# Optimization experiments

Hardware: AMD Instinct MI355X
Metric: run time of the kernel (lower is better)

## Reference

```python
import jax, jax.numpy as jnp
import numpy as np

EPS_RMS = 1.1920929e-07  # torch.finfo(float32).eps, RMSNorm default when eps=None
EPS_BN = 1e-5            # BatchNorm1d default eps
NUM_CODES = 4096
EMBED_DIM = 64


def rms_norm(x):
    # nn.RMSNorm(embed_dim, elementwise_affine=False)
    ms = jnp.mean(x * x, axis=-1, keepdims=True)
    return x * jax.lax.rsqrt(ms + EPS_RMS)


def get_codebook(codebook_weight, bn_weight, bn_bias):
    # BatchNorm1d with track_running_stats=False: batch stats over codebook rows
    mean = jnp.mean(codebook_weight, axis=0)
    var = jnp.var(codebook_weight, axis=0)  # biased variance, as torch BN uses
    h = (codebook_weight - mean) * jax.lax.rsqrt(var + EPS_BN) * bn_weight + bn_bias
    return rms_norm(h)


def setup_inputs() -> dict:
    key = jax.random.key(0)
    k1, k2 = jax.random.split(key)
    z = jax.random.normal(k1, (8, 4096, EMBED_DIM), dtype=jnp.float32)
    # codebook init: uniform(-1/num_codes, 1/num_codes)
    codebook_weight = jax.random.uniform(
        k2, (NUM_CODES, EMBED_DIM), dtype=jnp.float32,
        minval=-1.0 / NUM_CODES, maxval=1.0 / NUM_CODES)
    bn_weight = jnp.ones((EMBED_DIM,), dtype=jnp.float32)
    bn_bias = jnp.zeros((EMBED_DIM,), dtype=jnp.float32)
    return {"z": z, "codebook_weight": codebook_weight,
            "bn_weight": bn_weight, "bn_bias": bn_bias}


def reference(z, codebook_weight, bn_weight, bn_bias):
    # c_in / c_out are Identity since width == embed_dim
    z_e = rms_norm(z)                                   # [B, S, D]
    cb = get_codebook(codebook_weight, bn_weight, bn_bias)  # [K, D]

    z_flat = z_e.reshape(-1, z_e.shape[-1])             # [N, D]
    # argmin of cdist == argmin of squared distance (sqrt is monotone)
    d2 = (jnp.sum(z_flat * z_flat, axis=1, keepdims=True)
          - 2.0 * (z_flat @ cb.T)
          + jnp.sum(cb * cb, axis=1))                   # [N, K]
    q = jnp.argmin(d2, axis=1)                          # [N]

    z_q = cb[q].reshape(z_e.shape)                      # gather codes
    q = q.reshape(z_e.shape[:-1])

    # straight-through: gradient flows to z_e only
    z_q_st = z_e + jax.lax.stop_gradient(z_q - z_e)
    # ret_dict entries: 'z' (detached z_e), 'q', 'z_q' (detached)
    return (z_q_st, jax.lax.stop_gradient(z_e), q, jax.lax.stop_gradient(z_q))
```

## Files before the change

kernel.cpp:

```cpp
#include <hip/hip_runtime.h>
#include <math.h>

#define NROWS 32768
#define DIM   64
#define NCODE 4096
#define EPS_RMS 1.1920929e-07f
#define EPS_BN  1e-5f

typedef _Float16 f16x8 __attribute__((ext_vector_type(8)));
typedef float    f32x4 __attribute__((ext_vector_type(4)));

#define WS_PS   0
#define WS_PQ   16384
#define WS_CC   32768
#define WS_CB32 49152
#define WS_CH   (49152 + 1048576)
#define WS_CL   (WS_CH + 524288)

#define OUT1 ((size_t)NROWS * DIM)
#define OUT2 ((size_t)2 * NROWS * DIM)
#define OUT3 (OUT2 + NROWS)

#define MFMA16(a, b, c) __builtin_amdgcn_mfma_f32_16x16x32_f16(a, b, c, 0, 0, 0)

__device__ __forceinline__ void async_copy16(void* lds, const void* g) {
    __builtin_amdgcn_global_load_lds(
        (const __attribute__((address_space(1))) unsigned int*)g,
        (__attribute__((address_space(3))) unsigned int*)lds, 16, 0, 0);
}

__global__ __launch_bounds__(256) void k_bn1(const float* __restrict__ w,
                                             char* __restrict__ wsb) {
    __shared__ float s1[4][64], s2[4][64];
    int lane = threadIdx.x & 63, v = threadIdx.x >> 6;
    long base = (long)blockIdx.x * 64 + v * 16;
    float s = 0.f, sq = 0.f;
    #pragma unroll
    for (int i = 0; i < 16; i++) {
        float x = w[(base + i) * DIM + lane];
        s += x; sq += x * x;
    }
    s1[v][lane] = s; s2[v][lane] = sq;
    __syncthreads();
    if (threadIdx.x < 64) {
        float ts = s1[0][lane] + s1[1][lane] + s1[2][lane] + s1[3][lane];
        float tq = s2[0][lane] + s2[1][lane] + s2[2][lane] + s2[3][lane];
        ((float*)(wsb + WS_PS))[blockIdx.x * 64 + lane] = ts;
        ((float*)(wsb + WS_PQ))[blockIdx.x * 64 + lane] = tq;
    }
}

__global__ __launch_bounds__(256) void k_cb(const float* __restrict__ w,
                                            const float* __restrict__ bnw,
                                            const float* __restrict__ bnb,
                                            char* __restrict__ wsb) {
    __shared__ float s1[4][64], s2[4][64], af[64], bf[64];
    int t = threadIdx.x, lane = t & 63, v = t >> 6;
    const float* ps = (const float*)(wsb + WS_PS);
    const float* pq = (const float*)(wsb + WS_PQ);
    float s = 0.f, sq = 0.f;
    #pragma unroll
    for (int b = 0; b < 16; b++) {
        s  += ps[(v * 16 + b) * 64 + lane];
        sq += pq[(v * 16 + b) * 64 + lane];
    }
    s1[v][lane] = s; s2[v][lane] = sq;
    __syncthreads();
    if (t < 64) {
        float ts = s1[0][lane] + s1[1][lane] + s1[2][lane] + s1[3][lane];
        float tq = s2[0][lane] + s2[1][lane] + s2[2][lane] + s2[3][lane];
        float mean = ts * (1.0f / NCODE);
        float var  = tq * (1.0f / NCODE) - mean * mean;
        float a = rsqrtf(var + EPS_BN) * bnw[lane];
        af[lane] = a;
        bf[lane] = bnb[lane] - mean * a;
    }
    __syncthreads();
    float a = af[lane], bb = bf[lane];
    float*     cb32 = (float*)(wsb + WS_CB32);
    _Float16*  chG  = (_Float16*)(wsb + WS_CH);
    _Float16*  clG  = (_Float16*)(wsb + WS_CL);
    float*     ccp  = (float*)(wsb + WS_CC);
    #pragma unroll
    for (int i = 0; i < 4; i++) {
        long row = (long)blockIdx.x * 16 + v * 4 + i;
        float x = w[row * DIM + lane];
        float h = fmaf(x, a, bb);
        float ss = h * h;
        #pragma unroll
        for (int m = 1; m < 64; m <<= 1) ss += __shfl_xor(ss, m);
        float rms = rsqrtf(ss * (1.0f / DIM) + EPS_RMS);
        float c = h * rms;
        cb32[row * DIM + lane] = c;
        _Float16 ch = (_Float16)c;
        chG[row * DIM + lane] = ch;
        clG[row * DIM + lane] = (_Float16)(c - (float)ch);
        float cs = c * c;
        #pragma unroll
        for (int m = 1; m < 64; m <<= 1) cs += __shfl_xor(cs, m);
        if (lane == 0) ccp[row] = cs;
    }
}

__global__ __launch_bounds__(256, 2) void k_main(const float* __restrict__ z,
                                                 const char* __restrict__ wsb,
                                                 float* __restrict__ out) {
    __shared__ __align__(16) unsigned char sm[32768];
    unsigned char* chT = sm;
    unsigned char* clT = sm + 16384;

    const int tid  = threadIdx.x;
    const int lane = tid & 63;
    const int w    = tid >> 6;
    const int wr   = w >> 1;
    const int wc   = w & 1;
    const int l15  = lane & 15;
    const int l4   = lane >> 4;
    const long rowbase = (long)blockIdx.x * 64;

    const _Float16* chG  = (const _Float16*)(wsb + WS_CH);
    const _Float16* clG  = (const _Float16*)(wsb + WS_CL);
    const float*    ccG  = (const float*)(wsb + WS_CC);
    const float*    cb32 = (const float*)(wsb + WS_CB32);

    {
        int r = tid >> 2, seg = tid & 3;
        const float* zrow = z + (rowbase + r) * DIM + seg * 16;
        float vv[16];
        float ss = 0.f;
        #pragma unroll
        for (int i = 0; i < 16; i++) { vv[i] = zrow[i]; ss += vv[i] * vv[i]; }
        ss += __shfl_xor(ss, 1);
        ss += __shfl_xor(ss, 2);
        float rms = rsqrtf(ss * (1.0f / DIM) + EPS_RMS);
        float* oz = out + OUT1 + (rowbase + r) * DIM + seg * 16;
        __align__(16) _Float16 hb[16], lb[16];
        #pragma unroll
        for (int i = 0; i < 16; i++) {
            float x = vv[i] * rms;
            oz[i] = x;
            _Float16 h = (_Float16)x;
            hb[i] = h;
            lb[i] = (_Float16)(x - (float)h);
        }
        unsigned char* zhp = sm + r * 128 + seg * 32;
        unsigned char* zlp = sm + 8192 + r * 128 + seg * 32;
        ((f16x8*)zhp)[0] = ((f16x8*)hb)[0];
        ((f16x8*)zhp)[1] = ((f16x8*)hb)[1];
        ((f16x8*)zlp)[0] = ((f16x8*)lb)[0];
        ((f16x8*)zlp)[1] = ((f16x8*)lb)[1];
    }
    __syncthreads();

    f16x8 ah[2][2], al[2][2];
    #pragma unroll
    for (int s = 0; s < 2; s++)
        #pragma unroll
        for (int c = 0; c < 2; c++) {
            int arow = wr * 32 + s * 16 + l15;
            ah[s][c] = *(const f16x8*)(sm + arow * 128 + c * 64 + l4 * 16);
            al[s][c] = *(const f16x8*)(sm + 8192 + arow * 128 + c * 64 + l4 * 16);
        }
    __syncthreads();

    float bd[2][4];
    int   bix[2][4];
    #pragma unroll
    for (int s = 0; s < 2; s++)
        #pragma unroll
        for (int r = 0; r < 4; r++) { bd[s][r] = 3.4e38f; bix[s][r] = 0; }

    for (int p = 0; p < 32; ++p) {
        int cbase = p * 128;
        #pragma unroll
        for (int i = 0; i < 4; i++) {
            int B = w * 4096 + i * 1024 + lane * 16;
            int code = B >> 7;
            int sp   = (B >> 4) & 7;
            long ge = (long)(cbase + code) * DIM + (long)((sp ^ (code & 7)) * 8);
            async_copy16(chT + w * 4096 + i * 1024, chG + ge);
            async_copy16(clT + w * 4096 + i * 1024, clG + ge);
        }
        float ccv[4];
        #pragma unroll
        for (int q = 0; q < 4; q++)
            ccv[q] = ccG[cbase + wc * 64 + q * 16 + l15];
        __syncthreads();

        #pragma unroll 2
        for (int q = 0; q < 4; q++) {
            int ccol = wc * 64 + q * 16;
            int coderow = ccol + l15;
            f16x8 bh[2], bl[2];
            #pragma unroll
            for (int c = 0; c < 2; c++) {
                int byte = coderow * 128 + ((c * 64 + l4 * 16) ^ ((coderow & 7) << 4));
                bh[c] = *(const f16x8*)(chT + byte);
                bl[c] = *(const f16x8*)(clT + byte);
            }
            #pragma unroll
            for (int s = 0; s < 2; s++) {
                f32x4 acc = {0.f, 0.f, 0.f, 0.f};
                acc = MFMA16(ah[s][0], bh[0], acc);
                acc = MFMA16(ah[s][1], bh[1], acc);
                acc = MFMA16(ah[s][0], bl[0], acc);
                acc = MFMA16(ah[s][1], bl[1], acc);
                acc = MFMA16(al[s][0], bh[0], acc);
                acc = MFMA16(al[s][1], bh[1], acc);
                int code = cbase + ccol + l15;
                #pragma unroll
                for (int r = 0; r < 4; r++) {
                    float cand = fmaf(-2.0f, acc[r], ccv[q]);
                    if (cand < bd[s][r]) { bd[s][r] = cand; bix[s][r] = code; }
                }
            }
        }
        __syncthreads();
    }

    float* redd = (float*)sm;
    int*   redi = (int*)(sm + 512);
    int*   bidx = (int*)(sm + 1024);
    #pragma unroll
    for (int s = 0; s < 2; s++)
        #pragma unroll
        for (int r = 0; r < 4; r++) {
            float d = bd[s][r];
            int   ix = bix[s][r];
            #pragma unroll
            for (int m = 1; m < 16; m <<= 1) {
                float od = __shfl_xor(d, m);
                int   oi = __shfl_xor(ix, m);
                if (od < d || (od == d && oi < ix)) { d = od; ix = oi; }
            }
            if (l15 == 0) {
                int rowloc = wr * 32 + s * 16 + l4 * 4 + r;
                redd[rowloc * 2 + wc] = d;
                redi[rowloc * 2 + wc] = ix;
            }
        }
    __syncthreads();
    if (tid < 64) {
        float d0 = redd[tid * 2 + 0], d1 = redd[tid * 2 + 1];
        int   i0 = redi[tid * 2 + 0], i1 = redi[tid * 2 + 1];
        int ix = (d1 < d0 || (d1 == d0 && i1 < i0)) ? i1 : i0;
        bidx[tid] = ix;
        out[OUT2 + rowbase + tid] = (float)ix;
    }
    __syncthreads();
    {
        int r = tid >> 2, seg = tid & 3;
        int ix = bidx[r];
        const float* src = cb32 + (long)ix * DIM + seg * 16;
        float* o0 = out + (rowbase + r) * DIM + seg * 16;
        float* o3 = out + OUT3 + (rowbase + r) * DIM + seg * 16;
        #pragma unroll
        for (int i = 0; i < 16; i++) { float t = src[i]; o0[i] = t; o3[i] = t; }
    }
}

extern "C" void kernel_launch(void* const* d_in, const int* in_sizes, int n_in,
                              void* d_out, int out_size, void* d_ws, size_t ws_size,
                              hipStream_t stream) {
    const float* z   = (const float*)d_in[0];
    const float* w   = (const float*)d_in[1];
    const float* bnw = (const float*)d_in[2];
    const float* bnb = (const float*)d_in[3];
    float* out = (float*)d_out;
    char*  wsb = (char*)d_ws;

    k_bn1 <<<64,   256, 0, stream>>>(w, wsb);
    k_cb  <<<256,  256, 0, stream>>>(w, bnw, bnb, wsb);
    k_main<<<512,  256, 0, stream>>>(z, wsb, out);
}
```

Before: 84.37 us.

## Double-buffer codebook tiles in LDS and fold the code-norm term into MFMA

The main kernel now keeps two 32 KB LDS buffers for the fp16 hi/lo codebook tiles. It issues async copies for tile p+1, and its norm values, before computing on tile p, so global-to-LDS transfer overlaps the MFMA work and one barrier per iteration goes away. The distance is rewritten as an argmax of dot minus half the code norm, with the scaled norm precomputed by the codebook kernel and used as the MFMA accumulator initializer. The six-MFMA dependency chain is split into two independent chains, and the swizzled LDS offsets are hoisted out of the loop. LDS use per block doubles to 64 KB, which may reduce how many blocks fit per CU.

New measurement: 87.66 us. 3.9% more time.

```diff
diff --git a/kernel.cpp b/kernel.cpp
--- a/kernel.cpp
+++ b/kernel.cpp
@@ -98,16 +98,14 @@
         float cs = c * c;
         #pragma unroll
         for (int m = 1; m < 64; m <<= 1) cs += __shfl_xor(cs, m);
-        if (lane == 0) ccp[row] = cs;
+        if (lane == 0) ccp[row] = -0.5f * cs;
     }
 }
 
 __global__ __launch_bounds__(256, 2) void k_main(const float* __restrict__ z,
                                                  const char* __restrict__ wsb,
                                                  float* __restrict__ out) {
-    __shared__ __align__(16) unsigned char sm[32768];
-    unsigned char* chT = sm;
-    unsigned char* clT = sm + 16384;
+    __shared__ __align__(16) unsigned char sm[65536];
 
     const int tid  = threadIdx.x;
     const int lane = tid & 63;
@@ -120,8 +118,22 @@
 
     const _Float16* chG  = (const _Float16*)(wsb + WS_CH);
     const _Float16* clG  = (const _Float16*)(wsb + WS_CL);
-    const float*    ccG  = (const float*)(wsb + WS_CC);
+    const float*    ccnG = (const float*)(wsb + WS_CC);
     const float*    cb32 = (const float*)(wsb + WS_CB32);
+
+    const int B0    = w * 4096 + lane * 16;
+    const int scode = B0 >> 7;
+    const int ssp   = (B0 >> 4) & 7;
+    const long gsw  = (long)scode * DIM + (long)((ssp ^ (scode & 7)) * 8);
+
+    #pragma unroll
+    for (int i = 0; i < 4; i++) {
+        async_copy16(sm + B0 + i * 1024,         chG + gsw + i * 8 * DIM / 8 * 8);
+    }
+    #pragma unroll
+    for (int i = 0; i < 4; i++) {
+        async_copy16(sm + 16384 + B0 + i * 1024, clG + gsw + i * 8 * DIM / 8 * 8);
+    }
 
     {
         int r = tid >> 2, seg = tid & 3;
@@ -143,8 +155,8 @@
             hb[i] = h;
             lb[i] = (_Float16)(x - (float)h);
         }
-        unsigned char* zhp = sm + r * 128 + seg * 32;
-        unsigned char* zlp = sm + 8192 + r * 128 + seg * 32;
+        unsigned char* zhp = sm + 32768 + r * 128 + seg * 32;
+        unsigned char* zlp = sm + 40960 + r * 128 + seg * 32;
         ((f16x8*)zhp)[0] = ((f16x8*)hb)[0];
         ((f16x8*)zhp)[1] = ((f16x8*)hb)[1];
         ((f16x8*)zlp)[0] = ((f16x8*)lb)[0];
@@ -158,64 +170,82 @@
         #pragma unroll
         for (int c = 0; c < 2; c++) {
             int arow = wr * 32 + s * 16 + l15;
-            ah[s][c] = *(const f16x8*)(sm + arow * 128 + c * 64 + l4 * 16);
-            al[s][c] = *(const f16x8*)(sm + 8192 + arow * 128 + c * 64 + l4 * 16);
-        }
-    __syncthreads();
-
-    float bd[2][4];
+            ah[s][c] = *(const f16x8*)(sm + 32768 + arow * 128 + c * 64 + l4 * 16);
+            al[s][c] = *(const f16x8*)(sm + 40960 + arow * 128 + c * 64 + l4 * 16);
+        }
+    __syncthreads();
+
+    int boff[4][2];
+    #pragma unroll
+    for (int q = 0; q < 4; q++) {
+        int coderow = wc * 64 + q * 16 + l15;
+        #pragma unroll
+        for (int c = 0; c < 2; c++)
+            boff[q][c] = coderow * 128 + ((c * 64 + l4 * 16) ^ ((coderow & 7) << 4));
+    }
+
+    float ccv[4];
+    #pragma unroll
+    for (int q = 0; q < 4; q++)
+        ccv[q] = ccnG[wc * 64 + q * 16 + l15];
+
+    float bmax[2][4];
     int   bix[2][4];
     #pragma unroll
     for (int s = 0; s < 2; s++)
         #pragma unroll
-        for (int r = 0; r < 4; r++) { bd[s][r] = 3.4e38f; bix[s][r] = 0; }
+        for (int r = 0; r < 4; r++) { bmax[s][r] = -3.4e38f; bix[s][r] = 0; }
 
     for (int p = 0; p < 32; ++p) {
-        int cbase = p * 128;
-        #pragma unroll
-        for (int i = 0; i < 4; i++) {
-            int B = w * 4096 + i * 1024 + lane * 16;
-            int code = B >> 7;
-            int sp   = (B >> 4) & 7;
-            long ge = (long)(cbase + code) * DIM + (long)((sp ^ (code & 7)) * 8);
-            async_copy16(chT + w * 4096 + i * 1024, chG + ge);
-            async_copy16(clT + w * 4096 + i * 1024, clG + ge);
-        }
-        float ccv[4];
-        #pragma unroll
-        for (int q = 0; q < 4; q++)
-            ccv[q] = ccG[cbase + wc * 64 + q * 16 + l15];
-        __syncthreads();
+        float ccn_nx[4];
+        if (p + 1 < 32) {
+            const float* cn = ccnG + (p + 1) * 128;
+            #pragma unroll
+            for (int q = 0; q < 4; q++)
+                ccn_nx[q] = cn[wc * 64 + q * 16 + l15];
+            unsigned char* nb = sm + ((p + 1) & 1) * 32768;
+            const _Float16* gh = chG + (long)(p + 1) * 128 * DIM + gsw;
+            const _Float16* gl = clG + (long)(p + 1) * 128 * DIM + gsw;
+            #pragma unroll
+            for (int i = 0; i < 4; i++)
+                async_copy16(nb + B0 + i * 1024,         gh + i * 512);
+            #pragma unroll
+            for (int i = 0; i < 4; i++)
+                async_copy16(nb + 16384 + B0 + i * 1024, gl + i * 512);
+        }
+
+        const unsigned char* chT = sm + (p & 1) * 32768;
+        const unsigned char* clT = chT + 16384;
 
         #pragma unroll 2
         for (int q = 0; q < 4; q++) {
-            int ccol = wc * 64 + q * 16;
-            int coderow = ccol + l15;
             f16x8 bh[2], bl[2];
             #pragma unroll
             for (int c = 0; c < 2; c++) {
-                int byte = coderow * 128 + ((c * 64 + l4 * 16) ^ ((coderow & 7) << 4));
-                bh[c] = *(const f16x8*)(chT + byte);
-                bl[c] = *(const f16x8*)(clT + byte);
+                bh[c] = *(const f16x8*)(chT + boff[q][c]);
+                bl[c] = *(const f16x8*)(clT + boff[q][c]);
             }
+            int code = p * 128 + wc * 64 + q * 16 + l15;
+            f32x4 ci = {ccv[q], ccv[q], ccv[q], ccv[q]};
             #pragma unroll
             for (int s = 0; s < 2; s++) {
-                f32x4 acc = {0.f, 0.f, 0.f, 0.f};
-                acc = MFMA16(ah[s][0], bh[0], acc);
-                acc = MFMA16(ah[s][1], bh[1], acc);
-                acc = MFMA16(ah[s][0], bl[0], acc);
-                acc = MFMA16(ah[s][1], bl[1], acc);
-                acc = MFMA16(al[s][0], bh[0], acc);
-                acc = MFMA16(al[s][1], bh[1], acc);
-                int code = cbase + ccol + l15;
+                f32x4 a0 = MFMA16(ah[s][0], bh[0], ci);
+                a0 = MFMA16(ah[s][0], bl[0], a0);
+                a0 = MFMA16(al[s][0], bh[0], a0);
+                f32x4 zz = {0.f, 0.f, 0.f, 0.f};
+                f32x4 a1 = MFMA16(ah[s][1], bh[1], zz);
+                a1 = MFMA16(ah[s][1], bl[1], a1);
+                a1 = MFMA16(al[s][1], bh[1], a1);
                 #pragma unroll
                 for (int r = 0; r < 4; r++) {
-                    float cand = fmaf(-2.0f, acc[r], ccv[q]);
-                    if (cand < bd[s][r]) { bd[s][r] = cand; bix[s][r] = code; }
+                    float v = a0[r] + a1[r];
+                    if (v > bmax[s][r]) { bmax[s][r] = v; bix[s][r] = code; }
                 }
             }
         }
         __syncthreads();
+        #pragma unroll
+        for (int q = 0; q < 4; q++) ccv[q] = ccn_nx[q];
     }
 
     float* redd = (float*)sm;
@@ -225,13 +255,13 @@
     for (int s = 0; s < 2; s++)
         #pragma unroll
         for (int r = 0; r < 4; r++) {
-            float d = bd[s][r];
+            float d = bmax[s][r];
             int   ix = bix[s][r];
             #pragma unroll
             for (int m = 1; m < 16; m <<= 1) {
                 float od = __shfl_xor(d, m);
                 int   oi = __shfl_xor(ix, m);
-                if (od < d || (od == d && oi < ix)) { d = od; ix = oi; }
+                if (od > d || (od == d && oi < ix)) { d = od; ix = oi; }
             }
             if (l15 == 0) {
                 int rowloc = wr * 32 + s * 16 + l4 * 4 + r;
@@ -243,7 +273,7 @@
     if (tid < 64) {
         float d0 = redd[tid * 2 + 0], d1 = redd[tid * 2 + 1];
         int   i0 = redi[tid * 2 + 0], i1 = redi[tid * 2 + 1];
-        int ix = (d1 < d0 || (d1 == d0 && i1 < i0)) ? i1 : i0;
+        int ix = (d1 > d0 || (d1 == d0 && i1 < i0)) ? i1 : i0;
         bidx[tid] = ix;
         out[OUT2 + rowbase + tid] = (float)ix;
     }
@@ -269,7 +299,7 @@
     float* out = (float*)d_out;
     char*  wsb = (char*)d_ws;
 
-    k_bn1 <<<64,   256, 0, stream>>>(w, wsb);
-    k_cb  <<<256,  256, 0, stream>>>(w, bnw, bnb, wsb);
-    k_main<<<512,  256, 0, stream>>>(z, wsb, out);
-}
+    k_bn1 <<<64,  256, 0, stream>>>(w, wsb);
+    k_cb  <<<256, 256, 0, stream>>>(w, bnw, bnb, wsb);
+    k_main<<<512, 256, 0, stream>>>(z, wsb, out);
+}
```

## Prepack codebook into MFMA fragment layout and stream from global per wave

Applied to the files above, without the earlier changes.

The codebook kernel now writes fp16 hi/lo codes already arranged in MFMA B-fragment order, along with a precomputed -0.5*||c||^2 bias. The main kernel drops the LDS staging loop and its per-tile barriers. Each wave loads its fragments straight from global memory with double-buffered registers, covering 1024 codes for all 64 rows, and seeds the accumulator with the bias so it can take a running max. This removes LDS traffic and synchronisation and raises occupancy to 3 blocks per SM. In exchange, each wave re-reads the codebook from L2 for every block, and per-thread register use rises. The z and gather I/O is also vectorised to float4.

Measured after the change: 70.26 us (median of 2 runs). -16.7%, faster.

```diff
diff --git a/kernel.cpp b/kernel.cpp
--- a/kernel.cpp
+++ b/kernel.cpp
@@ -14,20 +14,14 @@
 #define WS_PQ   16384
 #define WS_CC   32768
 #define WS_CB32 49152
-#define WS_CH   (49152 + 1048576)
-#define WS_CL   (WS_CH + 524288)
+#define WS_PH   (49152 + 1048576)
+#define WS_PL   (WS_PH + 524288)
 
 #define OUT1 ((size_t)NROWS * DIM)
 #define OUT2 ((size_t)2 * NROWS * DIM)
 #define OUT3 (OUT2 + NROWS)
 
 #define MFMA16(a, b, c) __builtin_amdgcn_mfma_f32_16x16x32_f16(a, b, c, 0, 0, 0)
-
-__device__ __forceinline__ void async_copy16(void* lds, const void* g) {
-    __builtin_amdgcn_global_load_lds(
-        (const __attribute__((address_space(1))) unsigned int*)g,
-        (__attribute__((address_space(3))) unsigned int*)lds, 16, 0, 0);
-}
 
 __global__ __launch_bounds__(256) void k_bn1(const float* __restrict__ w,
                                              char* __restrict__ wsb) {
@@ -55,6 +49,7 @@
                                             const float* __restrict__ bnb,
                                             char* __restrict__ wsb) {
     __shared__ float s1[4][64], s2[4][64], af[64], bf[64];
+    __shared__ _Float16 sh[16][64], sl[16][64];
     int t = threadIdx.x, lane = t & 63, v = t >> 6;
     const float* ps = (const float*)(wsb + WS_PS);
     const float* pq = (const float*)(wsb + WS_PQ);
@@ -77,13 +72,13 @@
     }
     __syncthreads();
     float a = af[lane], bb = bf[lane];
-    float*     cb32 = (float*)(wsb + WS_CB32);
-    _Float16*  chG  = (_Float16*)(wsb + WS_CH);
-    _Float16*  clG  = (_Float16*)(wsb + WS_CL);
-    float*     ccp  = (float*)(wsb + WS_CC);
+    float* cb32 = (float*)(wsb + WS_CB32);
+    float* ccp  = (float*)(wsb + WS_CC);
+    int g = blockIdx.x;
     #pragma unroll
     for (int i = 0; i < 4; i++) {
-        long row = (long)blockIdx.x * 16 + v * 4 + i;
+        int  rl  = v * 4 + i;
+        long row = (long)g * 16 + rl;
         float x = w[row * DIM + lane];
         float h = fmaf(x, a, bb);
         float ss = h * h;
@@ -93,169 +88,185 @@
         float c = h * rms;
         cb32[row * DIM + lane] = c;
         _Float16 ch = (_Float16)c;
-        chG[row * DIM + lane] = ch;
-        clG[row * DIM + lane] = (_Float16)(c - (float)ch);
+        sh[rl][lane] = ch;
+        sl[rl][lane] = (_Float16)(c - (float)ch);
         float cs = c * c;
         #pragma unroll
         for (int m = 1; m < 64; m <<= 1) cs += __shfl_xor(cs, m);
-        if (lane == 0) ccp[row] = cs;
-    }
-}
-
-__global__ __launch_bounds__(256, 2) void k_main(const float* __restrict__ z,
+        if (lane == 0) ccp[row] = -0.5f * cs;
+    }
+    __syncthreads();
+    {
+        int u = t & 127;
+        int c = u >> 6, l = u & 63;
+        int codel = l & 15;
+        int kbase = c * 32 + (l >> 4) * 8;
+        size_t dst = (size_t)((g * 2 + c) * 64 + l) * 16;
+        if (t < 128) {
+            *(f16x8*)(wsb + WS_PH + dst) = *(const f16x8*)&sh[codel][kbase];
+        } else {
+            *(f16x8*)(wsb + WS_PL + dst) = *(const f16x8*)&sl[codel][kbase];
+        }
+    }
+}
+
+__global__ __launch_bounds__(256, 3) void k_main(const float* __restrict__ z,
                                                  const char* __restrict__ wsb,
                                                  float* __restrict__ out) {
-    __shared__ __align__(16) unsigned char sm[32768];
-    unsigned char* chT = sm;
-    unsigned char* clT = sm + 16384;
+    __shared__ __align__(16) unsigned char sm[18688];
 
     const int tid  = threadIdx.x;
     const int lane = tid & 63;
     const int w    = tid >> 6;
-    const int wr   = w >> 1;
-    const int wc   = w & 1;
     const int l15  = lane & 15;
     const int l4   = lane >> 4;
     const long rowbase = (long)blockIdx.x * 64;
 
-    const _Float16* chG  = (const _Float16*)(wsb + WS_CH);
-    const _Float16* clG  = (const _Float16*)(wsb + WS_CL);
-    const float*    ccG  = (const float*)(wsb + WS_CC);
-    const float*    cb32 = (const float*)(wsb + WS_CB32);
+    const float* ccnG = (const float*)(wsb + WS_CC);
+    const float* cb32 = (const float*)(wsb + WS_CB32);
 
     {
         int r = tid >> 2, seg = tid & 3;
-        const float* zrow = z + (rowbase + r) * DIM + seg * 16;
-        float vv[16];
+        const float4* zp = (const float4*)(z + (rowbase + r) * DIM + seg * 16);
+        float4 v4[4];
         float ss = 0.f;
         #pragma unroll
-        for (int i = 0; i < 16; i++) { vv[i] = zrow[i]; ss += vv[i] * vv[i]; }
+        for (int i = 0; i < 4; i++) {
+            v4[i] = zp[i];
+            ss += v4[i].x * v4[i].x + v4[i].y * v4[i].y + v4[i].z * v4[i].z + v4[i].w * v4[i].w;
+        }
         ss += __shfl_xor(ss, 1);
         ss += __shfl_xor(ss, 2);
         float rms = rsqrtf(ss * (1.0f / DIM) + EPS_RMS);
-        float* oz = out + OUT1 + (rowbase + r) * DIM + seg * 16;
+        float4* oz = (float4*)(out + OUT1 + (rowbase + r) * DIM + seg * 16);
         __align__(16) _Float16 hb[16], lb[16];
         #pragma unroll
-        for (int i = 0; i < 16; i++) {
-            float x = vv[i] * rms;
-            oz[i] = x;
-            _Float16 h = (_Float16)x;
-            hb[i] = h;
-            lb[i] = (_Float16)(x - (float)h);
+        for (int i = 0; i < 4; i++) {
+            float xs[4] = {v4[i].x, v4[i].y, v4[i].z, v4[i].w};
+            #pragma unroll
+            for (int j = 0; j < 4; j++) {
+                float x = xs[j] * rms;
+                _Float16 h = (_Float16)x;
+                hb[i * 4 + j] = h;
+                lb[i * 4 + j] = (_Float16)(x - (float)h);
+                xs[j] = x;
+            }
+            oz[i] = make_float4(xs[0], xs[1], xs[2], xs[3]);
         }
         unsigned char* zhp = sm + r * 128 + seg * 32;
-        unsigned char* zlp = sm + 8192 + r * 128 + seg * 32;
         ((f16x8*)zhp)[0] = ((f16x8*)hb)[0];
         ((f16x8*)zhp)[1] = ((f16x8*)hb)[1];
+        unsigned char* zlp = zhp + 8192;
         ((f16x8*)zlp)[0] = ((f16x8*)lb)[0];
         ((f16x8*)zlp)[1] = ((f16x8*)lb)[1];
     }
     __syncthreads();
 
-    f16x8 ah[2][2], al[2][2];
-    #pragma unroll
-    for (int s = 0; s < 2; s++)
+    f16x8 ah[4][2], al[4][2];
+    #pragma unroll
+    for (int s = 0; s < 4; s++)
         #pragma unroll
         for (int c = 0; c < 2; c++) {
-            int arow = wr * 32 + s * 16 + l15;
-            ah[s][c] = *(const f16x8*)(sm + arow * 128 + c * 64 + l4 * 16);
-            al[s][c] = *(const f16x8*)(sm + 8192 + arow * 128 + c * 64 + l4 * 16);
-        }
-    __syncthreads();
-
-    float bd[2][4];
-    int   bix[2][4];
-    #pragma unroll
-    for (int s = 0; s < 2; s++)
-        #pragma unroll
-        for (int r = 0; r < 4; r++) { bd[s][r] = 3.4e38f; bix[s][r] = 0; }
-
-    for (int p = 0; p < 32; ++p) {
-        int cbase = p * 128;
-        #pragma unroll
-        for (int i = 0; i < 4; i++) {
-            int B = w * 4096 + i * 1024 + lane * 16;
-            int code = B >> 7;
-            int sp   = (B >> 4) & 7;
-            long ge = (long)(cbase + code) * DIM + (long)((sp ^ (code & 7)) * 8);
-            async_copy16(chT + w * 4096 + i * 1024, chG + ge);
-            async_copy16(clT + w * 4096 + i * 1024, clG + ge);
-        }
-        float ccv[4];
-        #pragma unroll
-        for (int q = 0; q < 4; q++)
-            ccv[q] = ccG[cbase + wc * 64 + q * 16 + l15];
-        __syncthreads();
-
-        #pragma unroll 2
-        for (int q = 0; q < 4; q++) {
-            int ccol = wc * 64 + q * 16;
-            int coderow = ccol + l15;
-            f16x8 bh[2], bl[2];
-            #pragma unroll
-            for (int c = 0; c < 2; c++) {
-                int byte = coderow * 128 + ((c * 64 + l4 * 16) ^ ((coderow & 7) << 4));
-                bh[c] = *(const f16x8*)(chT + byte);
-                bl[c] = *(const f16x8*)(clT + byte);
-            }
-            #pragma unroll
-            for (int s = 0; s < 2; s++) {
-                f32x4 acc = {0.f, 0.f, 0.f, 0.f};
-                acc = MFMA16(ah[s][0], bh[0], acc);
-                acc = MFMA16(ah[s][1], bh[1], acc);
-                acc = MFMA16(ah[s][0], bl[0], acc);
-                acc = MFMA16(ah[s][1], bl[1], acc);
-                acc = MFMA16(al[s][0], bh[0], acc);
-                acc = MFMA16(al[s][1], bh[1], acc);
-                int code = cbase + ccol + l15;
-                #pragma unroll
-                for (int r = 0; r < 4; r++) {
-                    float cand = fmaf(-2.0f, acc[r], ccv[q]);
-                    if (cand < bd[s][r]) { bd[s][r] = cand; bix[s][r] = code; }
-                }
-            }
-        }
-        __syncthreads();
-    }
-
-    float* redd = (float*)sm;
-    int*   redi = (int*)(sm + 512);
-    int*   bidx = (int*)(sm + 1024);
-    #pragma unroll
-    for (int s = 0; s < 2; s++)
+            int off = (s * 16 + l15) * 128 + c * 64 + l4 * 16;
+            ah[s][c] = *(const f16x8*)(sm + off);
+            al[s][c] = *(const f16x8*)(sm + 8192 + off);
+        }
+
+    float bmax[4][4];
+    int   bix[4][4];
+    #pragma unroll
+    for (int s = 0; s < 4; s++)
+        #pragma unroll
+        for (int r = 0; r < 4; r++) { bmax[s][r] = -3.4e38f; bix[s][r] = 0; }
+
+    const int gw = w * 64;
+    const char* pH = wsb + WS_PH + (size_t)(gw * 2) * 1024 + lane * 16;
+    const char* pL = wsb + WS_PL + (size_t)(gw * 2) * 1024 + lane * 16;
+    const float* cn = ccnG + gw * 16 + l15;
+
+    #define LOADB(H0, H1, L0, L1, CC, k)                       \
+        H0 = *(const f16x8*)(pH + (size_t)(k) * 2048);         \
+        H1 = *(const f16x8*)(pH + (size_t)(k) * 2048 + 1024);  \
+        L0 = *(const f16x8*)(pL + (size_t)(k) * 2048);         \
+        L1 = *(const f16x8*)(pL + (size_t)(k) * 2048 + 1024);  \
+        CC = cn[(k) * 16];
+
+    #define COMPUTE(H0, H1, L0, L1, CC, k)                                        \
+    {                                                                             \
+        int code = (gw + (k)) * 16 + l15;                                         \
+        _Pragma("unroll")                                                         \
+        for (int s = 0; s < 4; s++) {                                             \
+            f32x4 a2 = {CC, CC, CC, CC};                                          \
+            a2 = MFMA16(ah[s][0], H0, a2);                                        \
+            a2 = MFMA16(ah[s][1], H1, a2);                                        \
+            a2 = MFMA16(ah[s][0], L0, a2);                                        \
+            a2 = MFMA16(ah[s][1], L1, a2);                                        \
+            a2 = MFMA16(al[s][0], H0, a2);                                        \
+            a2 = MFMA16(al[s][1], H1, a2);                                        \
+            _Pragma("unroll")                                                     \
+            for (int r = 0; r < 4; r++) {                                         \
+                if (a2[r] > bmax[s][r]) { bmax[s][r] = a2[r]; bix[s][r] = code; } \
+            }                                                                     \
+        }                                                                         \
+    }
+
+    f16x8 hA0, hA1, lA0, lA1, hB0, hB1, lB0, lB1;
+    float ccA, ccB;
+    LOADB(hA0, hA1, lA0, lA1, ccA, 0);
+    #pragma unroll 1
+    for (int k = 0; k < 62; k += 2) {
+        LOADB(hB0, hB1, lB0, lB1, ccB, k + 1);
+        COMPUTE(hA0, hA1, lA0, lA1, ccA, k);
+        LOADB(hA0, hA1, lA0, lA1, ccA, k + 2);
+        COMPUTE(hB0, hB1, lB0, lB1, ccB, k + 1);
+    }
+    LOADB(hB0, hB1, lB0, lB1, ccB, 63);
+    COMPUTE(hA0, hA1, lA0, lA1, ccA, 62);
+    COMPUTE(hB0, hB1, lB0, lB1, ccB, 63);
+
+    float* redd = (float*)(sm + 16384);
+    int*   redi = (int*)(sm + 17408);
+    int*   bidx = (int*)(sm + 18432);
+    #pragma unroll
+    for (int s = 0; s < 4; s++)
         #pragma unroll
         for (int r = 0; r < 4; r++) {
-            float d = bd[s][r];
+            float d = bmax[s][r];
             int   ix = bix[s][r];
             #pragma unroll
             for (int m = 1; m < 16; m <<= 1) {
                 float od = __shfl_xor(d, m);
                 int   oi = __shfl_xor(ix, m);
-                if (od < d || (od == d && oi < ix)) { d = od; ix = oi; }
+                if (od > d || (od == d && oi < ix)) { d = od; ix = oi; }
             }
             if (l15 == 0) {
-                int rowloc = wr * 32 + s * 16 + l4 * 4 + r;
-                redd[rowloc * 2 + wc] = d;
-                redi[rowloc * 2 + wc] = ix;
+                int row = s * 16 + l4 * 4 + r;
+                redd[row * 4 + w] = d;
+                redi[row * 4 + w] = ix;
             }
         }
     __syncthreads();
     if (tid < 64) {
-        float d0 = redd[tid * 2 + 0], d1 = redd[tid * 2 + 1];
-        int   i0 = redi[tid * 2 + 0], i1 = redi[tid * 2 + 1];
-        int ix = (d1 < d0 || (d1 == d0 && i1 < i0)) ? i1 : i0;
-        bidx[tid] = ix;
-        out[OUT2 + rowbase + tid] = (float)ix;
+        float bv = redd[tid * 4];
+        int   bi_ = redi[tid * 4];
+        #pragma unroll
+        for (int j = 1; j < 4; j++) {
+            float dj = redd[tid * 4 + j];
+            int   ij = redi[tid * 4 + j];
+            if (dj > bv || (dj == bv && ij < bi_)) { bv = dj; bi_ = ij; }
+        }
+        bidx[tid] = bi_;
+        out[OUT2 + rowbase + tid] = (float)bi_;
     }
     __syncthreads();
     {
         int r = tid >> 2, seg = tid & 3;
         int ix = bidx[r];
-        const float* src = cb32 + (long)ix * DIM + seg * 16;
-        float* o0 = out + (rowbase + r) * DIM + seg * 16;
-        float* o3 = out + OUT3 + (rowbase + r) * DIM + seg * 16;
-        #pragma unroll
-        for (int i = 0; i < 16; i++) { float t = src[i]; o0[i] = t; o3[i] = t; }
+        const float4* src = (const float4*)(cb32 + (long)ix * DIM + seg * 16);
+        float4* o0 = (float4*)(out + (rowbase + r) * DIM + seg * 16);
+        float4* o3 = (float4*)(out + OUT3 + (rowbase + r) * DIM + seg * 16);
+        #pragma unroll
+        for (int i = 0; i < 4; i++) { float4 t4 = src[i]; o0[i] = t4; o3[i] = t4; }
     }
 }
 
@@ -269,7 +280,7 @@
     float* out = (float*)d_out;
     char*  wsb = (char*)d_ws;
 
-    k_bn1 <<<64,   256, 0, stream>>>(w, wsb);
-    k_cb  <<<256,  256, 0, stream>>>(w, bnw, bnb, wsb);
-    k_main<<<512,  256, 0, stream>>>(z, wsb, out);
-}
+    k_bn1 <<<64,  256, 0, stream>>>(w, wsb);
+    k_cb  <<<256, 256, 0, stream>>>(w, bnw, bnb, wsb);
+    k_main<<<512, 256, 0, stream>>>(z, wsb, out);
+}
```
